# Kernel optimization log

Hardware: AMD Instinct MI355X
Metric: run time of the kernel (lower is better)

The kernel has to match this reference:

```python
import jax, jax.numpy as jnp
import numpy as np

B = 256            # number of graphs
N_NODES = 512      # nodes per graph
D = 128            # embedding_dim = hidden_dim
NUM_EDGE_CLASSES = 8
N_TOTAL = B * N_NODES
N_EDGES = N_TOTAL * 8   # avg degree 8
EDGES_DIM = N_NODES * (N_NODES - 1) // 2


def _ln(x, g, b):
    m = jnp.mean(x, axis=-1, keepdims=True)
    v = jnp.var(x, axis=-1, keepdims=True)
    return (x - m) * jax.lax.rsqrt(v + 1e-5) * g + b


def _mlp_ln(x, W1, b1, g, be, W2, b2):
    # MLP(input,hidden,output, n_hidden_layers=1, add_layer_norm=True):
    # Linear -> LayerNorm -> ReLU -> Linear
    return jax.nn.relu(_ln(x @ W1 + b1, g, be)) @ W2 + b2


def setup_inputs() -> dict:
    key = jax.random.key(0)
    ks = jax.random.split(key, 12)
    s = 1.0 / np.sqrt(D)
    return {
        "node_features": jax.random.randint(ks[0], (N_TOTAL, 1), 0, N_NODES),
        "edge_index": jax.random.randint(ks[1], (2, N_EDGES), 0, N_TOTAL),
        "batch_ptr": jnp.arange(B + 1, dtype=jnp.int32) * N_NODES,
        "emb": jax.random.normal(ks[2], (N_NODES, D), jnp.float32) * 0.02,
        "gin_W1": jax.random.normal(ks[3], (D, D), jnp.float32) * s,
        "gin_b1": jnp.zeros((D,), jnp.float32),
        "gin_g1": jnp.ones((D,), jnp.float32),
        "gin_be1": jnp.zeros((D,), jnp.float32),
        "gin_W2": jax.random.normal(ks[4], (D, D), jnp.float32) * s,
        "gin_b2": jnp.zeros((D,), jnp.float32),
        "post_W1": jax.random.normal(ks[5], (D, D), jnp.float32) * s,
        "post_b1": jnp.zeros((D,), jnp.float32),
        "post_W2": jax.random.normal(ks[6], (D, D), jnp.float32) * s,
        "post_b2": jnp.zeros((D,), jnp.float32),
        "norm_g": jnp.ones((D,), jnp.float32),
        "norm_b": jnp.zeros((D,), jnp.float32),
        "exit_W1": jax.random.normal(ks[7], (D, D), jnp.float32) * s,
        "exit_b1": jnp.zeros((D,), jnp.float32),
        "exit_g": jnp.ones((D,), jnp.float32),
        "exit_be": jnp.zeros((D,), jnp.float32),
        "exit_W2": jax.random.normal(ks[8], (D, 1), jnp.float32) * s,
        "exit_b2": jnp.zeros((1,), jnp.float32),
    }


def reference(node_features, edge_index, batch_ptr, emb,
              gin_W1, gin_b1, gin_g1, gin_be1, gin_W2, gin_b2,
              post_W1, post_b1, post_W2, post_b2,
              norm_g, norm_b,
              exit_W1, exit_b1, exit_g, exit_be, exit_W2, exit_b2):
    # node embedding lookup
    x = emb[node_features.squeeze(-1)]                      # [N_total, D]

    # single GIN conv layer (eps=0): MLP(x + sum_{j in N(i)} x_j)
    src, dst = edge_index[0], edge_index[1]
    agg = jax.ops.segment_sum(x[src], dst, num_segments=N_TOTAL)
    h = _mlp_ln(x + agg, gin_W1, gin_b1, gin_g1, gin_be1, gin_W2, gin_b2)
    # post-conv Sequential(Linear, ReLU, Linear)
    h = jax.nn.relu(h @ post_W1 + post_b1) @ post_W2 + post_b2
    # i == 0: no residual; then LayerNorm
    x = _ln(h, norm_g, norm_b)                              # [N_total, D]

    # segment mean via cumsum (faithful to _group_mean)
    cs = jnp.concatenate([jnp.zeros((1, D), x.dtype), jnp.cumsum(x, axis=0)], 0)
    sizes = (batch_ptr[1:] - batch_ptr[:-1]).astype(x.dtype)
    means = (cs[batch_ptr[1:]] - cs[batch_ptr[:-1]]) / sizes[:, None]  # [B, D]

    exit_action = _mlp_ln(means, exit_W1, exit_b1, exit_g, exit_be,
                          exit_W2, exit_b2).squeeze(-1)     # [B]

    # per-graph pairwise dot products, upper-triangular gather
    xb = x.reshape(B, N_NODES, D)
    scores = jnp.einsum('bnf,bmf->bnm', xb, xb) / jnp.sqrt(
        jnp.asarray(D, x.dtype))                            # [B, n, n]
    iu, ju = jnp.triu_indices(N_NODES, k=1)
    edge_actions = scores[:, iu, ju]                        # [B, EDGES_DIM]

    # action_type: index 1 = ADD_EDGE, 2 = EXIT (GraphActionType assumption)
    action_type = (jnp.zeros((B, 3), x.dtype)
                   .at[:, 1].set(1.0 - exit_action)
                   .at[:, 2].set(exit_action))
    edge_class = jnp.zeros((B, NUM_EDGE_CLASSES), x.dtype)
    node_class = jnp.zeros((B, 1), x.dtype)
    return (action_type, edge_class, node_class, edge_actions)
```

## Files before the change

kernel.cpp:

```cpp
#include <hip/hip_runtime.h>
#include <hip/hip_bf16.h>

#define NBATCH 256
#define NNODES 512
#define DIM    128
#define NTOT   (NBATCH*NNODES)
#define NEDGE  (NTOT*8)
#define EPB    130816
#define CAP    32

typedef __attribute__((ext_vector_type(8))) short  short8;
typedef __attribute__((ext_vector_type(4))) float  f32x4;

__device__ __forceinline__ unsigned short f2bf(float f){
  unsigned u = __builtin_bit_cast(unsigned, f);
  unsigned r = u + 0x7FFFu + ((u >> 16) & 1u);
  return (unsigned short)(r >> 16);
}

__global__ __launch_bounds__(256) void k_prep(
    const float* __restrict__ emb, const float* __restrict__ W1,
    unsigned short* __restrict__ embW1,
    const float* __restrict__ W2, const float* __restrict__ P1,
    const float* __restrict__ P2, unsigned short* __restrict__ wswz,
    int* __restrict__ cnt, float* __restrict__ gsum, float* __restrict__ out)
{
  const int tid = threadIdx.x;
  const int blk = blockIdx.x;
  __shared__ float er[2][DIM];
  if (blk < 256) {
    const int half = tid >> 7, c = tid & 127;
    const int r = blk*2 + half;
    er[half][c] = emb[r*DIM + c];
    __syncthreads();
    float acc = 0.f;
    #pragma unroll 8
    for (int k = 0; k < DIM; ++k) acc = fmaf(er[half][k], W1[k*DIM + c], acc);
    embW1[r*DIM + c] = f2bf(acc);
  } else if (blk < 448) {
    int idx = (blk - 256)*256 + tid;
    int s = idx >> 14, rem = idx & 16383;
    int ks = rem >> 12, n = (rem >> 9) & 7, lane = (rem >> 3) & 63, j = rem & 7;
    int lg = lane >> 4, l15 = lane & 15;
    int k = ks*32 + lg*8 + j, c = n*16 + l15;
    const float* src = (s == 0) ? W2 : ((s == 1) ? P1 : P2);
    wswz[idx] = f2bf(src[k*DIM + c]);
  } else {
    int idx = (blk - 448)*256 + tid;
    if (idx < NTOT)                cnt[idx] = 0;
    else if (idx < NTOT + 32768)   gsum[idx - NTOT] = 0.f;
    else                           out[idx - NTOT - 32768] = 0.f;
  }
}

__global__ __launch_bounds__(256) void k_edges(const int* __restrict__ ei,
                                               const int* __restrict__ nf,
                                               int* __restrict__ cnt,
                                               unsigned short* __restrict__ slots){
  const int base = (blockIdx.x >> 3)*4096 + threadIdx.x;
  const int r    = blockIdx.x & 7;
  #pragma unroll
  for (int it = 0; it < 16; ++it) {
    const int e = base + it*256;
    const int d = ei[NEDGE + e];
    if ((d >> 14) == r) {
      const int s = ei[e];
      const int v = nf[s];
      const int pos = atomicAdd(&cnt[d], 1);
      if (pos < CAP) slots[(size_t)d*CAP + pos] = (unsigned short)v;
    }
  }
}

__global__ __launch_bounds__(512, 4) void k_gnn(
    const unsigned short* __restrict__ embW1, const int* __restrict__ nf,
    const int* __restrict__ cnt, const unsigned short* __restrict__ slots,
    const float* __restrict__ b1, const float* __restrict__ g1,
    const float* __restrict__ be1,
    const unsigned short* __restrict__ wswz,
    const float* __restrict__ b2,  const float* __restrict__ pb1, const float* __restrict__ pb2,
    const float* __restrict__ ng,  const float* __restrict__ nbv,
    unsigned short* __restrict__ xbuf, float* __restrict__ gsum)
{
  __shared__ unsigned short act[32][136];
  __shared__ float rpart[4][32][2];
  __shared__ float rfin[32][2];
  __shared__ float gpart[8][128];
  const int tid   = threadIdx.x;
  const int nbase = blockIdx.x * 32;

  {
    const int node = nbase + (tid >> 4);
    const int part = tid & 15;
    const short8* base8 = (const short8*)embW1;

    const int self = nf[node];
    int m = cnt[node]; if (m > CAP) m = CAP;
    const unsigned short* sl = slots + (size_t)node*CAP;
    const uint4 sv0 = *(const uint4*)(sl);
    const uint4 sv1 = *(const uint4*)(sl + 8);
    const uint4 sv2 = *(const uint4*)(sl + 16);
    unsigned sw[12] = {sv0.x,sv0.y,sv0.z,sv0.w, sv1.x,sv1.y,sv1.z,sv1.w,
                       sv2.x,sv2.y,sv2.z,sv2.w};

    float a[8];
    {
      const float4* bp = (const float4*)(b1 + part*8);
      float4 x = bp[0], y = bp[1];
      a[0]=x.x; a[1]=x.y; a[2]=x.z; a[3]=x.w;
      a[4]=y.x; a[5]=y.y; a[6]=y.z; a[7]=y.w;
    }
#define ACC8(V) { _Pragma("unroll") \
    for (int i_ = 0; i_ < 8; ++i_) { \
      unsigned uu = ((unsigned)(unsigned short)(V)[i_]) << 16; \
      a[i_] += __builtin_bit_cast(float, uu); } }

    {
      short8 t0 = base8[(size_t)self*16 + part];
      short8 t[8];
      #pragma unroll
      for (int e = 0; e < 8; ++e) {
        unsigned id = (sw[e >> 1] >> ((e & 1)*16)) & 0xffffu;
        int idx = (e < m) ? (int)id : self;
        t[e] = base8[(size_t)idx*16 + part];
      }
      ACC8(t0)
      #pragma unroll
      for (int e = 0; e < 8; ++e) if (e < m) ACC8(t[e])
    }
    if (m > 8) {
      short8 t[8];
      #pragma unroll
      for (int e = 0; e < 8; ++e) {
        unsigned id = (sw[4 + (e >> 1)] >> ((e & 1)*16)) & 0xffffu;
        int idx = (e + 8 < m) ? (int)id : self;
        t[e] = base8[(size_t)idx*16 + part];
      }
      #pragma unroll
      for (int e = 0; e < 8; ++e) if (e + 8 < m) ACC8(t[e])
    }
    if (m > 16) {
      short8 t[8];
      #pragma unroll
      for (int e = 0; e < 8; ++e) {
        unsigned id = (sw[8 + (e >> 1)] >> ((e & 1)*16)) & 0xffffu;
        int idx = (e + 16 < m) ? (int)id : self;
        t[e] = base8[(size_t)idx*16 + part];
      }
      #pragma unroll
      for (int e = 0; e < 8; ++e) if (e + 16 < m) ACC8(t[e])
    }
    for (int e = 24; e < m; ++e) {
      short8 t = base8[(size_t)sl[e]*16 + part];
      ACC8(t)
    }

    float s = 0.f, qs = 0.f;
    #pragma unroll
    for (int i = 0; i < 8; ++i) { s += a[i]; qs += a[i]*a[i]; }
    #pragma unroll
    for (int msk = 1; msk < 16; msk <<= 1) {
      s  += __shfl_xor(s,  msk, 64);
      qs += __shfl_xor(qs, msk, 64);
    }
    const float mean = s * (1.f/128.f);
    const float var  = qs * (1.f/128.f) - mean*mean;
    const float rs   = rsqrtf(var + 1e-5f);
    float gg[8], bb[8];
    {
      const float4* gp = (const float4*)(g1  + part*8);
      const float4* ep = (const float4*)(be1 + part*8);
      float4 g0 = gp[0], g1v = gp[1], e0 = ep[0], e1v = ep[1];
      gg[0]=g0.x; gg[1]=g0.y; gg[2]=g0.z; gg[3]=g0.w;
      gg[4]=g1v.x; gg[5]=g1v.y; gg[6]=g1v.z; gg[7]=g1v.w;
      bb[0]=e0.x; bb[1]=e0.y; bb[2]=e0.z; bb[3]=e0.w;
      bb[4]=e1v.x; bb[5]=e1v.y; bb[6]=e1v.z; bb[7]=e1v.w;
    }
    float v[8];
    #pragma unroll
    for (int i = 0; i < 8; ++i)
      v[i] = fmaxf((a[i] - mean)*rs*gg[i] + bb[i], 0.f);
    uint4 pk;
    pk.x = (unsigned)f2bf(v[0]) | ((unsigned)f2bf(v[1]) << 16);
    pk.y = (unsigned)f2bf(v[2]) | ((unsigned)f2bf(v[3]) << 16);
    pk.z = (unsigned)f2bf(v[4]) | ((unsigned)f2bf(v[5]) << 16);
    pk.w = (unsigned)f2bf(v[6]) | ((unsigned)f2bf(v[7]) << 16);
    *(uint4*)&act[tid >> 4][part*8] = pk;
  }
  __syncthreads();

  const int wave = tid >> 6, lane = tid & 63;
  const int l15 = lane & 15, lg = lane >> 4;
  const int rt = wave & 1, nb = wave >> 1;
  const int arow = rt*16 + l15;
  const short8* ws8 = (const short8*)wswz;

  for (int s = 0; s < 3; ++s) {
    f32x4 acc0 = (f32x4){0.f,0.f,0.f,0.f};
    f32x4 acc1 = (f32x4){0.f,0.f,0.f,0.f};
    #pragma unroll
    for (int ks = 0; ks < 4; ++ks) {
      short8 af  = *(const short8*)&act[arow][ks*32 + lg*8];
      short8 bf0 = ws8[s*2048 + ks*512 + (nb*2 + 0)*64 + lane];
      short8 bf1 = ws8[s*2048 + ks*512 + (nb*2 + 1)*64 + lane];
      acc0 = __builtin_amdgcn_mfma_f32_16x16x32_bf16(af, bf0, acc0, 0, 0, 0);
      acc1 = __builtin_amdgcn_mfma_f32_16x16x32_bf16(af, bf1, acc1, 0, 0, 0);
    }
    __syncthreads();

    if (s < 2) {
      const float* bias = (s == 0) ? b2 : pb1;
      const float bb0 = bias[nb*32 + l15], bb1 = bias[nb*32 + 16 + l15];
      #pragma unroll
      for (int q = 0; q < 4; ++q) {
        float x0 = acc0[q] + bb0, x1 = acc1[q] + bb1;
        if (s == 1) { x0 = fmaxf(x0, 0.f); x1 = fmaxf(x1, 0.f); }
        act[rt*16 + lg*4 + q][nb*32 + l15]      = f2bf(x0);
        act[rt*16 + lg*4 + q][nb*32 + 16 + l15] = f2bf(x1);
      }
      __syncthreads();
    } else {
      const float bb0 = pb2[nb*32 + l15], bb1 = pb2[nb*32 + 16 + l15];
      float w0v[4], w1v[4], sr[4], qr[4];
      #pragma unroll
      for (int q = 0; q < 4; ++q) {
        float x0 = acc0[q] + bb0, x1 = acc1[q] + bb1;
        w0v[q] = x0; w1v[q] = x1;
        sr[q] = x0 + x1; qr[q] = x0*x0 + x1*x1;
      }
      #pragma unroll
      for (int msk = 1; msk < 16; msk <<= 1) {
        #pragma unroll
        for (int q = 0; q < 4; ++q) {
          sr[q] += __shfl_xor(sr[q], msk, 64);
          qr[q] += __shfl_xor(qr[q], msk, 64);
        }
      }
      if (l15 == 0) {
        #pragma unroll
        for (int q = 0; q < 4; ++q) {
          rpart[nb][rt*16 + lg*4 + q][0] = sr[q];
          rpart[nb][rt*16 + lg*4 + q][1] = qr[q];
        }
      }
      __syncthreads();
      if (tid < 64) {
        int row = tid >> 1, vv = tid & 1;
        rfin[row][vv] = rpart[0][row][vv] + rpart[1][row][vv]
                      + rpart[2][row][vv] + rpart[3][row][vv];
      }
      __syncthreads();
      const int c0 = nb*32 + l15, c1 = c0 + 16;
      const float gc0 = ng[c0], gc1 = ng[c1], bc0 = nbv[c0], bc1 = nbv[c1];
      float pc0 = 0.f, pc1 = 0.f;
      #pragma unroll
      for (int q = 0; q < 4; ++q) {
        const int row = rt*16 + lg*4 + q;
        const float mean = rfin[row][0]*(1.f/128.f);
        const float var  = rfin[row][1]*(1.f/128.f) - mean*mean;
        const float rs   = rsqrtf(var + 1e-5f);
        float x0 = (w0v[q] - mean)*rs*gc0 + bc0;
        float x1 = (w1v[q] - mean)*rs*gc1 + bc1;
        act[row][c0] = f2bf(x0);
        act[row][c1] = f2bf(x1);
        pc0 += x0; pc1 += x1;
      }
      pc0 += __shfl_xor(pc0, 16, 64); pc0 += __shfl_xor(pc0, 32, 64);
      pc1 += __shfl_xor(pc1, 16, 64); pc1 += __shfl_xor(pc1, 32, 64);
      if (lg == 0) { gpart[wave][c0] = pc0; gpart[wave][c1] = pc1; }
      __syncthreads();
      if (tid < 128) {
        const int w0 = (tid >> 5)*2;
        float s2 = gpart[w0][tid] + gpart[w0 + 1][tid];
        atomicAdd(&gsum[(blockIdx.x >> 4)*DIM + tid], s2);
      }
      {
        short8* xs8 = (short8*)xbuf;
        const int i = tid;
        const int rowgrp = i >> 8, rem = i & 255;
        const int kc = rem >> 4, lv = rem & 15;
        short8 vv = *(const short8*)&act[rowgrp*16 + lv][kc*8];
        xs8[((size_t)(nbase >> 4) + rowgrp)*256 + kc*16 + lv] = vv;
      }
    }
  }
}

__global__ __launch_bounds__(256) void k_scores(const unsigned short* __restrict__ xswz,
    const float* __restrict__ gsum,
    const float* __restrict__ eW1, const float* __restrict__ eb1,
    const float* __restrict__ eg,  const float* __restrict__ ebe,
    const float* __restrict__ eW2, const float* __restrict__ eb2,
    float* __restrict__ out)
{
  const int tid = threadIdx.x;

  if (blockIdx.x >= 2560) {
    __shared__ float mrow[2][DIM];
    __shared__ float red[2][2][2];
    __shared__ float red2[2][2];
    const int grp = tid >> 7;
    const int t   = tid & 127;
    const int gi  = ((int)blockIdx.x - 2560)*2 + grp;
    mrow[grp][t] = gsum[gi*DIM + t] * (1.f/512.f);
    __syncthreads();
    float u = eb1[t];
    #pragma unroll 8
    for (int k = 0; k < DIM; ++k) u = fmaf(mrow[grp][k], eW1[k*DIM + t], u);
    float s = u, q = u*u;
    #pragma unroll
    for (int m = 1; m < 64; m <<= 1) { s += __shfl_xor(s, m, 64); q += __shfl_xor(q, m, 64); }
    const int wv = (tid >> 6) & 1;
    if ((tid & 63) == 0) { red[grp][wv][0] = s; red[grp][wv][1] = q; }
    __syncthreads();
    const float S = red[grp][0][0] + red[grp][1][0];
    const float Q = red[grp][0][1] + red[grp][1][1];
    const float mean = S*(1.f/128.f);
    const float var  = Q*(1.f/128.f) - mean*mean;
    float av = fmaxf((u - mean)*rsqrtf(var + 1e-5f)*eg[t] + ebe[t], 0.f);
    float p = av * eW2[t];
    #pragma unroll
    for (int m = 1; m < 64; m <<= 1) p += __shfl_xor(p, m, 64);
    if ((tid & 63) == 0) red2[grp][wv] = p;
    __syncthreads();
    if (t == 0) {
      float e = red2[grp][0] + red2[grp][1] + eb2[0];
      out[gi*3 + 1] = 1.f - e;
      out[gi*3 + 2] = e;
    }
    return;
  }

  static const int TI[10] = {0,0,0,0,1,1,1,2,2,3};
  static const int TJ[10] = {0,1,2,3,1,2,3,2,3,3};
  const int b = blockIdx.x & 255, p = blockIdx.x >> 8;
  const int ti = TI[p], tj = TJ[p];
  const int wave = tid >> 6, lane = tid & 63;
  const int l15 = lane & 15, lg = lane >> 4;
  const short8* Xs = (const short8*)xswz + (size_t)b*8192;

  f32x4 acc0[8], acc1[8];
  #pragma unroll
  for (int n = 0; n < 8; ++n) { acc0[n] = (f32x4){0,0,0,0}; acc1[n] = (f32x4){0,0,0,0}; }

  #pragma unroll
  for (int ks = 0; ks < 4; ++ks) {
    const int kq = ks*4 + lg;
    short8 a0 = Xs[(size_t)(ti*8 + wave*2 + 0)*256 + kq*16 + l15];
    short8 a1 = Xs[(size_t)(ti*8 + wave*2 + 1)*256 + kq*16 + l15];
    #pragma unroll
    for (int n = 0; n < 8; ++n) {
      short8 bf = Xs[(size_t)(tj*8 + n)*256 + kq*16 + l15];
      acc0[n] = __builtin_amdgcn_mfma_f32_16x16x32_bf16(a0, bf, acc0[n], 0, 0, 0);
      acc1[n] = __builtin_amdgcn_mfma_f32_16x16x32_bf16(a1, bf, acc1[n], 0, 0, 0);
    }
  }

  const float scale = 0.08838834764831845f;
  float* ea = out + 3072 + (size_t)b*EPB;
  #pragma unroll
  for (int m = 0; m < 2; ++m) {
    #pragma unroll
    for (int n = 0; n < 8; ++n) {
      const int gj = tj*128 + n*16 + l15;
      #pragma unroll
      for (int r = 0; r < 4; ++r) {
        const int gi = ti*128 + wave*32 + m*16 + lg*4 + r;
        if (gi < gj) {
          const int rowbase = gi*511 - (gi*(gi-1))/2 - gi - 1;
          const float v = (m == 0) ? acc0[n][r] : acc1[n][r];
          ea[rowbase + gj] = v * scale;
        }
      }
    }
  }
}

extern "C" void kernel_launch(void* const* d_in, const int* in_sizes, int n_in,
                              void* d_out, int out_size, void* d_ws, size_t ws_size,
                              hipStream_t stream) {
  const int*   nf   = (const int*)d_in[0];
  const int*   ei   = (const int*)d_in[1];
  const float* emb  = (const float*)d_in[3];
  const float* gW1  = (const float*)d_in[4];
  const float* gb1  = (const float*)d_in[5];
  const float* gg1  = (const float*)d_in[6];
  const float* gbe1 = (const float*)d_in[7];
  const float* gW2  = (const float*)d_in[8];
  const float* gb2  = (const float*)d_in[9];
  const float* pW1  = (const float*)d_in[10];
  const float* pb1  = (const float*)d_in[11];
  const float* pW2  = (const float*)d_in[12];
  const float* pb2  = (const float*)d_in[13];
  const float* ng   = (const float*)d_in[14];
  const float* nb   = (const float*)d_in[15];
  const float* eW1  = (const float*)d_in[16];
  const float* eb1  = (const float*)d_in[17];
  const float* eg   = (const float*)d_in[18];
  const float* ebe  = (const float*)d_in[19];
  const float* eW2  = (const float*)d_in[20];
  const float* eb2  = (const float*)d_in[21];
  float* out = (float*)d_out;

  char* ws = (char*)d_ws;
  unsigned short* embW1 = (unsigned short*)ws;
  unsigned short* wswz  = (unsigned short*)(ws + 262144);
  int*            cnt   = (int*)(ws + 360448);
  unsigned short* slots = (unsigned short*)(ws + 884736);
  unsigned short* xbuf  = (unsigned short*)(ws + 13467648);
  float*          gsum  = (float*)(ws + 47022080);
  if (ws_size < 47153152) return;

  k_prep  <<<1100, 256, 0, stream>>>(emb, gW1, embW1, gW2, pW1, pW2, wswz,
                                     cnt, gsum, out);
  k_edges <<<2048, 256, 0, stream>>>(ei, nf, cnt, slots);
  k_gnn   <<<4096, 512, 0, stream>>>(embW1, nf, cnt, slots, gb1, gg1, gbe1,
                                     wswz, gb2, pb1, pb2, ng, nb, xbuf, gsum);
  k_scores<<<2688, 256, 0, stream>>>(xbuf, gsum, eW1, eb1, eg, ebe, eW2, eb2, out);
}
```

Measured before the change: 164.9 us.

## Fuse GNN MLP, graph mean, exit head and pairwise scores into one per-graph kernel

Merges k_gnn and k_scores into a single kernel that runs one 512-thread block per graph. Each block keeps all 512 node embeddings in shared memory (about 136 KB), runs the three MLP stages over the whole graph, reduces the graph mean locally instead of with global atomics, evaluates the exit head, and computes the upper-triangular pairwise scores straight from shared memory. This removes the xbuf round trip through global memory, the gsum atomics and zeroing, and one launch. In exchange only 256 blocks run on the GPU, with heavy register and shared-memory use per block, so occupancy and parallelism drop sharply. Because the score phase is bound by output writes, that lost parallelism may cost more than the traffic saved.

```diff
diff --git a/kernel.cpp b/kernel.cpp
--- a/kernel.cpp
+++ b/kernel.cpp
@@ -23,7 +23,7 @@
     unsigned short* __restrict__ embW1,
     const float* __restrict__ W2, const float* __restrict__ P1,
     const float* __restrict__ P2, unsigned short* __restrict__ wswz,
-    int* __restrict__ cnt, float* __restrict__ gsum, float* __restrict__ out)
+    int* __restrict__ cnt)
 {
   const int tid = threadIdx.x;
   const int blk = blockIdx.x;
@@ -46,10 +46,7 @@
     const float* src = (s == 0) ? W2 : ((s == 1) ? P1 : P2);
     wswz[idx] = f2bf(src[k*DIM + c]);
   } else {
-    int idx = (blk - 448)*256 + tid;
-    if (idx < NTOT)                cnt[idx] = 0;
-    else if (idx < NTOT + 32768)   gsum[idx - NTOT] = 0.f;
-    else                           out[idx - NTOT - 32768] = 0.f;
+    cnt[(blk - 448)*256 + tid] = 0;
   }
 }
 
@@ -72,7 +69,7 @@
   }
 }
 
-__global__ __launch_bounds__(512, 4) void k_gnn(
+__global__ __launch_bounds__(512, 2) void k_mega(
     const unsigned short* __restrict__ embW1, const int* __restrict__ nf,
     const int* __restrict__ cnt, const unsigned short* __restrict__ slots,
     const float* __restrict__ b1, const float* __restrict__ g1,
@@ -80,296 +77,288 @@
     const unsigned short* __restrict__ wswz,
     const float* __restrict__ b2,  const float* __restrict__ pb1, const float* __restrict__ pb2,
     const float* __restrict__ ng,  const float* __restrict__ nbv,
-    unsigned short* __restrict__ xbuf, float* __restrict__ gsum)
-{
-  __shared__ unsigned short act[32][136];
-  __shared__ float rpart[4][32][2];
-  __shared__ float rfin[32][2];
-  __shared__ float gpart[8][128];
-  const int tid   = threadIdx.x;
-  const int nbase = blockIdx.x * 32;
-
-  {
-    const int node = nbase + (tid >> 4);
-    const int part = tid & 15;
-    const short8* base8 = (const short8*)embW1;
-
-    const int self = nf[node];
-    int m = cnt[node]; if (m > CAP) m = CAP;
-    const unsigned short* sl = slots + (size_t)node*CAP;
-    const uint4 sv0 = *(const uint4*)(sl);
-    const uint4 sv1 = *(const uint4*)(sl + 8);
-    const uint4 sv2 = *(const uint4*)(sl + 16);
-    unsigned sw[12] = {sv0.x,sv0.y,sv0.z,sv0.w, sv1.x,sv1.y,sv1.z,sv1.w,
-                       sv2.x,sv2.y,sv2.z,sv2.w};
-
-    float a[8];
-    {
-      const float4* bp = (const float4*)(b1 + part*8);
-      float4 x = bp[0], y = bp[1];
-      a[0]=x.x; a[1]=x.y; a[2]=x.z; a[3]=x.w;
-      a[4]=y.x; a[5]=y.y; a[6]=y.z; a[7]=y.w;
-    }
-#define ACC8(V) { _Pragma("unroll") \
-    for (int i_ = 0; i_ < 8; ++i_) { \
-      unsigned uu = ((unsigned)(unsigned short)(V)[i_]) << 16; \
-      a[i_] += __builtin_bit_cast(float, uu); } }
-
-    {
-      short8 t0 = base8[(size_t)self*16 + part];
-      short8 t[8];
-      #pragma unroll
-      for (int e = 0; e < 8; ++e) {
-        unsigned id = (sw[e >> 1] >> ((e & 1)*16)) & 0xffffu;
-        int idx = (e < m) ? (int)id : self;
-        t[e] = base8[(size_t)idx*16 + part];
-      }
-      ACC8(t0)
-      #pragma unroll
-      for (int e = 0; e < 8; ++e) if (e < m) ACC8(t[e])
-    }
-    if (m > 8) {
-      short8 t[8];
-      #pragma unroll
-      for (int e = 0; e < 8; ++e) {
-        unsigned id = (sw[4 + (e >> 1)] >> ((e & 1)*16)) & 0xffffu;
-        int idx = (e + 8 < m) ? (int)id : self;
-        t[e] = base8[(size_t)idx*16 + part];
-      }
-      #pragma unroll
-      for (int e = 0; e < 8; ++e) if (e + 8 < m) ACC8(t[e])
-    }
-    if (m > 16) {
-      short8 t[8];
-      #pragma unroll
-      for (int e = 0; e < 8; ++e) {
-        unsigned id = (sw[8 + (e >> 1)] >> ((e & 1)*16)) & 0xffffu;
-        int idx = (e + 16 < m) ? (int)id : self;
-        t[e] = base8[(size_t)idx*16 + part];
-      }
-      #pragma unroll
-      for (int e = 0; e < 8; ++e) if (e + 16 < m) ACC8(t[e])
-    }
-    for (int e = 24; e < m; ++e) {
-      short8 t = base8[(size_t)sl[e]*16 + part];
-      ACC8(t)
-    }
-
-    float s = 0.f, qs = 0.f;
-    #pragma unroll
-    for (int i = 0; i < 8; ++i) { s += a[i]; qs += a[i]*a[i]; }
-    #pragma unroll
-    for (int msk = 1; msk < 16; msk <<= 1) {
-      s  += __shfl_xor(s,  msk, 64);
-      qs += __shfl_xor(qs, msk, 64);
-    }
-    const float mean = s * (1.f/128.f);
-    const float var  = qs * (1.f/128.f) - mean*mean;
-    const float rs   = rsqrtf(var + 1e-5f);
-    float gg[8], bb[8];
-    {
-      const float4* gp = (const float4*)(g1  + part*8);
-      const float4* ep = (const float4*)(be1 + part*8);
-      float4 g0 = gp[0], g1v = gp[1], e0 = ep[0], e1v = ep[1];
-      gg[0]=g0.x; gg[1]=g0.y; gg[2]=g0.z; gg[3]=g0.w;
-      gg[4]=g1v.x; gg[5]=g1v.y; gg[6]=g1v.z; gg[7]=g1v.w;
-      bb[0]=e0.x; bb[1]=e0.y; bb[2]=e0.z; bb[3]=e0.w;
-      bb[4]=e1v.x; bb[5]=e1v.y; bb[6]=e1v.z; bb[7]=e1v.w;
-    }
-    float v[8];
-    #pragma unroll
-    for (int i = 0; i < 8; ++i)
-      v[i] = fmaxf((a[i] - mean)*rs*gg[i] + bb[i], 0.f);
-    uint4 pk;
-    pk.x = (unsigned)f2bf(v[0]) | ((unsigned)f2bf(v[1]) << 16);
-    pk.y = (unsigned)f2bf(v[2]) | ((unsigned)f2bf(v[3]) << 16);
-    pk.z = (unsigned)f2bf(v[4]) | ((unsigned)f2bf(v[5]) << 16);
-    pk.w = (unsigned)f2bf(v[6]) | ((unsigned)f2bf(v[7]) << 16);
-    *(uint4*)&act[tid >> 4][part*8] = pk;
-  }
-  __syncthreads();
-
-  const int wave = tid >> 6, lane = tid & 63;
-  const int l15 = lane & 15, lg = lane >> 4;
-  const int rt = wave & 1, nb = wave >> 1;
-  const int arow = rt*16 + l15;
-  const short8* ws8 = (const short8*)wswz;
-
-  for (int s = 0; s < 3; ++s) {
-    f32x4 acc0 = (f32x4){0.f,0.f,0.f,0.f};
-    f32x4 acc1 = (f32x4){0.f,0.f,0.f,0.f};
-    #pragma unroll
-    for (int ks = 0; ks < 4; ++ks) {
-      short8 af  = *(const short8*)&act[arow][ks*32 + lg*8];
-      short8 bf0 = ws8[s*2048 + ks*512 + (nb*2 + 0)*64 + lane];
-      short8 bf1 = ws8[s*2048 + ks*512 + (nb*2 + 1)*64 + lane];
-      acc0 = __builtin_amdgcn_mfma_f32_16x16x32_bf16(af, bf0, acc0, 0, 0, 0);
-      acc1 = __builtin_amdgcn_mfma_f32_16x16x32_bf16(af, bf1, acc1, 0, 0, 0);
-    }
-    __syncthreads();
-
-    if (s < 2) {
-      const float* bias = (s == 0) ? b2 : pb1;
-      const float bb0 = bias[nb*32 + l15], bb1 = bias[nb*32 + 16 + l15];
-      #pragma unroll
-      for (int q = 0; q < 4; ++q) {
-        float x0 = acc0[q] + bb0, x1 = acc1[q] + bb1;
-        if (s == 1) { x0 = fmaxf(x0, 0.f); x1 = fmaxf(x1, 0.f); }
-        act[rt*16 + lg*4 + q][nb*32 + l15]      = f2bf(x0);
-        act[rt*16 + lg*4 + q][nb*32 + 16 + l15] = f2bf(x1);
-      }
-      __syncthreads();
-    } else {
-      const float bb0 = pb2[nb*32 + l15], bb1 = pb2[nb*32 + 16 + l15];
-      float w0v[4], w1v[4], sr[4], qr[4];
-      #pragma unroll
-      for (int q = 0; q < 4; ++q) {
-        float x0 = acc0[q] + bb0, x1 = acc1[q] + bb1;
-        w0v[q] = x0; w1v[q] = x1;
-        sr[q] = x0 + x1; qr[q] = x0*x0 + x1*x1;
-      }
-      #pragma unroll
-      for (int msk = 1; msk < 16; msk <<= 1) {
-        #pragma unroll
-        for (int q = 0; q < 4; ++q) {
-          sr[q] += __shfl_xor(sr[q], msk, 64);
-          qr[q] += __shfl_xor(qr[q], msk, 64);
-        }
-      }
-      if (l15 == 0) {
-        #pragma unroll
-        for (int q = 0; q < 4; ++q) {
-          rpart[nb][rt*16 + lg*4 + q][0] = sr[q];
-          rpart[nb][rt*16 + lg*4 + q][1] = qr[q];
-        }
-      }
-      __syncthreads();
-      if (tid < 64) {
-        int row = tid >> 1, vv = tid & 1;
-        rfin[row][vv] = rpart[0][row][vv] + rpart[1][row][vv]
-                      + rpart[2][row][vv] + rpart[3][row][vv];
-      }
-      __syncthreads();
-      const int c0 = nb*32 + l15, c1 = c0 + 16;
-      const float gc0 = ng[c0], gc1 = ng[c1], bc0 = nbv[c0], bc1 = nbv[c1];
-      float pc0 = 0.f, pc1 = 0.f;
-      #pragma unroll
-      for (int q = 0; q < 4; ++q) {
-        const int row = rt*16 + lg*4 + q;
-        const float mean = rfin[row][0]*(1.f/128.f);
-        const float var  = rfin[row][1]*(1.f/128.f) - mean*mean;
-        const float rs   = rsqrtf(var + 1e-5f);
-        float x0 = (w0v[q] - mean)*rs*gc0 + bc0;
-        float x1 = (w1v[q] - mean)*rs*gc1 + bc1;
-        act[row][c0] = f2bf(x0);
-        act[row][c1] = f2bf(x1);
-        pc0 += x0; pc1 += x1;
-      }
-      pc0 += __shfl_xor(pc0, 16, 64); pc0 += __shfl_xor(pc0, 32, 64);
-      pc1 += __shfl_xor(pc1, 16, 64); pc1 += __shfl_xor(pc1, 32, 64);
-      if (lg == 0) { gpart[wave][c0] = pc0; gpart[wave][c1] = pc1; }
-      __syncthreads();
-      if (tid < 128) {
-        const int w0 = (tid >> 5)*2;
-        float s2 = gpart[w0][tid] + gpart[w0 + 1][tid];
-        atomicAdd(&gsum[(blockIdx.x >> 4)*DIM + tid], s2);
-      }
-      {
-        short8* xs8 = (short8*)xbuf;
-        const int i = tid;
-        const int rowgrp = i >> 8, rem = i & 255;
-        const int kc = rem >> 4, lv = rem & 15;
-        short8 vv = *(const short8*)&act[rowgrp*16 + lv][kc*8];
-        xs8[((size_t)(nbase >> 4) + rowgrp)*256 + kc*16 + lv] = vv;
-      }
-    }
-  }
-}
-
-__global__ __launch_bounds__(256) void k_scores(const unsigned short* __restrict__ xswz,
-    const float* __restrict__ gsum,
     const float* __restrict__ eW1, const float* __restrict__ eb1,
     const float* __restrict__ eg,  const float* __restrict__ ebe,
     const float* __restrict__ eW2, const float* __restrict__ eb2,
     float* __restrict__ out)
 {
-  const int tid = threadIdx.x;
-
-  if (blockIdx.x >= 2560) {
-    __shared__ float mrow[2][DIM];
-    __shared__ float red[2][2][2];
-    __shared__ float red2[2][2];
-    const int grp = tid >> 7;
-    const int t   = tid & 127;
-    const int gi  = ((int)blockIdx.x - 2560)*2 + grp;
-    mrow[grp][t] = gsum[gi*DIM + t] * (1.f/512.f);
-    __syncthreads();
-    float u = eb1[t];
+  __shared__ unsigned short X[512][136];
+  __shared__ float gpart[8][128];
+  __shared__ float mrow[128];
+  __shared__ float redA[4];
+  __shared__ float redB[2];
+  const int tid   = threadIdx.x;
+  const int bb    = blockIdx.x;
+  const int nbase = bb * NNODES;
+
+  {
+    const int part = tid & 15;
+    const short8* base8 = (const short8*)embW1;
+    #pragma unroll 1
+    for (int pass = 0; pass < 16; ++pass) {
+      const int lnode = pass*32 + (tid >> 4);
+      const int node  = nbase + lnode;
+      const int self = nf[node];
+      int m = cnt[node]; if (m > CAP) m = CAP;
+      const unsigned short* sl = slots + (size_t)node*CAP;
+      const uint4 sv0 = *(const uint4*)(sl);
+      const uint4 sv1 = *(const uint4*)(sl + 8);
+      const uint4 sv2 = *(const uint4*)(sl + 16);
+      unsigned sw[12] = {sv0.x,sv0.y,sv0.z,sv0.w, sv1.x,sv1.y,sv1.z,sv1.w,
+                         sv2.x,sv2.y,sv2.z,sv2.w};
+      float a[8];
+      {
+        const float4* bp = (const float4*)(b1 + part*8);
+        float4 x = bp[0], y = bp[1];
+        a[0]=x.x; a[1]=x.y; a[2]=x.z; a[3]=x.w;
+        a[4]=y.x; a[5]=y.y; a[6]=y.z; a[7]=y.w;
+      }
+#define ACC8(V) { _Pragma("unroll") \
+      for (int i_ = 0; i_ < 8; ++i_) { \
+        unsigned uu = ((unsigned)(unsigned short)(V)[i_]) << 16; \
+        a[i_] += __builtin_bit_cast(float, uu); } }
+      {
+        short8 t0 = base8[(size_t)self*16 + part];
+        short8 t[8];
+        #pragma unroll
+        for (int e = 0; e < 8; ++e) {
+          unsigned id = (sw[e >> 1] >> ((e & 1)*16)) & 0xffffu;
+          int idx = (e < m) ? (int)id : self;
+          t[e] = base8[(size_t)idx*16 + part];
+        }
+        ACC8(t0)
+        #pragma unroll
+        for (int e = 0; e < 8; ++e) if (e < m) ACC8(t[e])
+      }
+      if (m > 8) {
+        short8 t[8];
+        #pragma unroll
+        for (int e = 0; e < 8; ++e) {
+          unsigned id = (sw[4 + (e >> 1)] >> ((e & 1)*16)) & 0xffffu;
+          int idx = (e + 8 < m) ? (int)id : self;
+          t[e] = base8[(size_t)idx*16 + part];
+        }
+        #pragma unroll
+        for (int e = 0; e < 8; ++e) if (e + 8 < m) ACC8(t[e])
+      }
+      if (m > 16) {
+        short8 t[8];
+        #pragma unroll
+        for (int e = 0; e < 8; ++e) {
+          unsigned id = (sw[8 + (e >> 1)] >> ((e & 1)*16)) & 0xffffu;
+          int idx = (e + 16 < m) ? (int)id : self;
+          t[e] = base8[(size_t)idx*16 + part];
+        }
+        #pragma unroll
+        for (int e = 0; e < 8; ++e) if (e + 16 < m) ACC8(t[e])
+      }
+      for (int e = 24; e < m; ++e) {
+        short8 t = base8[(size_t)sl[e]*16 + part];
+        ACC8(t)
+      }
+      float s = 0.f, qs = 0.f;
+      #pragma unroll
+      for (int i = 0; i < 8; ++i) { s += a[i]; qs += a[i]*a[i]; }
+      #pragma unroll
+      for (int msk = 1; msk < 16; msk <<= 1) {
+        s  += __shfl_xor(s,  msk, 64);
+        qs += __shfl_xor(qs, msk, 64);
+      }
+      const float mean = s * (1.f/128.f);
+      const float var  = qs * (1.f/128.f) - mean*mean;
+      const float rs   = rsqrtf(var + 1e-5f);
+      const float4* gp = (const float4*)(g1  + part*8);
+      const float4* ep = (const float4*)(be1 + part*8);
+      float4 g0 = gp[0], g1v = gp[1], e0 = ep[0], e1v = ep[1];
+      float gg[8] = {g0.x,g0.y,g0.z,g0.w, g1v.x,g1v.y,g1v.z,g1v.w};
+      float eb[8] = {e0.x,e0.y,e0.z,e0.w, e1v.x,e1v.y,e1v.z,e1v.w};
+      float v[8];
+      #pragma unroll
+      for (int i = 0; i < 8; ++i)
+        v[i] = fmaxf((a[i] - mean)*rs*gg[i] + eb[i], 0.f);
+      uint4 pk;
+      pk.x = (unsigned)f2bf(v[0]) | ((unsigned)f2bf(v[1]) << 16);
+      pk.y = (unsigned)f2bf(v[2]) | ((unsigned)f2bf(v[3]) << 16);
+      pk.z = (unsigned)f2bf(v[4]) | ((unsigned)f2bf(v[5]) << 16);
+      pk.w = (unsigned)f2bf(v[6]) | ((unsigned)f2bf(v[7]) << 16);
+      *(uint4*)&X[lnode][part*8] = pk;
+    }
+  }
+  __syncthreads();
+
+  const int wave = tid >> 6, lane = tid & 63;
+  const int l15 = lane & 15, lg = lane >> 4;
+  const short8* ws8 = (const short8*)wswz;
+  float pc[8];
+  #pragma unroll
+  for (int n = 0; n < 8; ++n) pc[n] = 0.f;
+
+  #pragma unroll
+  for (int s = 0; s < 3; ++s) {
+    f32x4 acc[4][8];
+    #pragma unroll
+    for (int p4 = 0; p4 < 4; ++p4)
+      #pragma unroll
+      for (int n = 0; n < 8; ++n) acc[p4][n] = (f32x4){0.f,0.f,0.f,0.f};
+    #pragma unroll
+    for (int ks = 0; ks < 4; ++ks) {
+      short8 bf[8];
+      #pragma unroll
+      for (int n = 0; n < 8; ++n) bf[n] = ws8[s*2048 + ks*512 + n*64 + lane];
+      #pragma unroll
+      for (int p4 = 0; p4 < 4; ++p4) {
+        short8 af = *(const short8*)&X[p4*128 + wave*16 + l15][ks*32 + lg*8];
+        #pragma unroll
+        for (int n = 0; n < 8; ++n)
+          acc[p4][n] = __builtin_amdgcn_mfma_f32_16x16x32_bf16(af, bf[n], acc[p4][n], 0, 0, 0);
+      }
+    }
+    if (s < 2) {
+      const float* bias = (s == 0) ? b2 : pb1;
+      float bv[8];
+      #pragma unroll
+      for (int n = 0; n < 8; ++n) bv[n] = bias[n*16 + l15];
+      #pragma unroll
+      for (int p4 = 0; p4 < 4; ++p4)
+        #pragma unroll
+        for (int n = 0; n < 8; ++n)
+          #pragma unroll
+          for (int q = 0; q < 4; ++q) {
+            float v = acc[p4][n][q] + bv[n];
+            if (s == 1) v = fmaxf(v, 0.f);
+            X[p4*128 + wave*16 + lg*4 + q][n*16 + l15] = f2bf(v);
+          }
+    } else {
+      float bv[8], gc[8], bc[8];
+      #pragma unroll
+      for (int n = 0; n < 8; ++n) {
+        bv[n] = pb2[n*16 + l15];
+        gc[n] = ng [n*16 + l15];
+        bc[n] = nbv[n*16 + l15];
+      }
+      #pragma unroll
+      for (int p4 = 0; p4 < 4; ++p4) {
+        float sr[4] = {0,0,0,0}, qr[4] = {0,0,0,0};
+        #pragma unroll
+        for (int n = 0; n < 8; ++n)
+          #pragma unroll
+          for (int q = 0; q < 4; ++q) {
+            float v = acc[p4][n][q] + bv[n];
+            acc[p4][n][q] = v;
+            sr[q] += v; qr[q] += v*v;
+          }
+        #pragma unroll
+        for (int msk = 1; msk < 16; msk <<= 1)
+          #pragma unroll
+          for (int q = 0; q < 4; ++q) {
+            sr[q] += __shfl_xor(sr[q], msk, 64);
+            qr[q] += __shfl_xor(qr[q], msk, 64);
+          }
+        float mean[4], rs[4];
+        #pragma unroll
+        for (int q = 0; q < 4; ++q) {
+          mean[q] = sr[q]*(1.f/128.f);
+          float var = qr[q]*(1.f/128.f) - mean[q]*mean[q];
+          rs[q] = rsqrtf(var + 1e-5f);
+        }
+        #pragma unroll
+        for (int n = 0; n < 8; ++n)
+          #pragma unroll
+          for (int q = 0; q < 4; ++q) {
+            float xo = (acc[p4][n][q] - mean[q])*rs[q]*gc[n] + bc[n];
+            X[p4*128 + wave*16 + lg*4 + q][n*16 + l15] = f2bf(xo);
+            pc[n] += xo;
+          }
+      }
+    }
+  }
+  #pragma unroll
+  for (int n = 0; n < 8; ++n) {
+    pc[n] += __shfl_xor(pc[n], 16, 64);
+    pc[n] += __shfl_xor(pc[n], 32, 64);
+  }
+  if (lg == 0) {
+    #pragma unroll
+    for (int n = 0; n < 8; ++n) gpart[wave][n*16 + l15] = pc[n];
+  }
+  __syncthreads();
+
+  if (tid < 128) {
+    float m = 0.f;
+    #pragma unroll
+    for (int w = 0; w < 8; ++w) m += gpart[w][tid];
+    mrow[tid] = m * (1.f/512.f);
+  }
+  __syncthreads();
+  float uu = 0.f;
+  if (tid < 128) {
+    uu = eb1[tid];
     #pragma unroll 8
-    for (int k = 0; k < DIM; ++k) u = fmaf(mrow[grp][k], eW1[k*DIM + t], u);
-    float s = u, q = u*u;
-    #pragma unroll
-    for (int m = 1; m < 64; m <<= 1) { s += __shfl_xor(s, m, 64); q += __shfl_xor(q, m, 64); }
-    const int wv = (tid >> 6) & 1;
-    if ((tid & 63) == 0) { red[grp][wv][0] = s; red[grp][wv][1] = q; }
-    __syncthreads();
-    const float S = red[grp][0][0] + red[grp][1][0];
-    const float Q = red[grp][0][1] + red[grp][1][1];
+    for (int k = 0; k < DIM; ++k) uu = fmaf(mrow[k], eW1[k*DIM + tid], uu);
+    float s2 = uu, q2 = uu*uu;
+    #pragma unroll
+    for (int msk = 1; msk < 64; msk <<= 1) {
+      s2 += __shfl_xor(s2, msk, 64); q2 += __shfl_xor(q2, msk, 64);
+    }
+    if ((tid & 63) == 0) { redA[(tid >> 6)*2] = s2; redA[(tid >> 6)*2 + 1] = q2; }
+  }
+  __syncthreads();
+  if (tid < 128) {
+    const float S = redA[0] + redA[2], Q = redA[1] + redA[3];
     const float mean = S*(1.f/128.f);
     const float var  = Q*(1.f/128.f) - mean*mean;
-    float av = fmaxf((u - mean)*rsqrtf(var + 1e-5f)*eg[t] + ebe[t], 0.f);
-    float p = av * eW2[t];
-    #pragma unroll
-    for (int m = 1; m < 64; m <<= 1) p += __shfl_xor(p, m, 64);
-    if ((tid & 63) == 0) red2[grp][wv] = p;
-    __syncthreads();
-    if (t == 0) {
-      float e = red2[grp][0] + red2[grp][1] + eb2[0];
-      out[gi*3 + 1] = 1.f - e;
-      out[gi*3 + 2] = e;
-    }
-    return;
-  }
-
-  static const int TI[10] = {0,0,0,0,1,1,1,2,2,3};
-  static const int TJ[10] = {0,1,2,3,1,2,3,2,3,3};
-  const int b = blockIdx.x & 255, p = blockIdx.x >> 8;
-  const int ti = TI[p], tj = TJ[p];
-  const int wave = tid >> 6, lane = tid & 63;
-  const int l15 = lane & 15, lg = lane >> 4;
-  const short8* Xs = (const short8*)xswz + (size_t)b*8192;
-
-  f32x4 acc0[8], acc1[8];
-  #pragma unroll
-  for (int n = 0; n < 8; ++n) { acc0[n] = (f32x4){0,0,0,0}; acc1[n] = (f32x4){0,0,0,0}; }
-
-  #pragma unroll
-  for (int ks = 0; ks < 4; ++ks) {
-    const int kq = ks*4 + lg;
-    short8 a0 = Xs[(size_t)(ti*8 + wave*2 + 0)*256 + kq*16 + l15];
-    short8 a1 = Xs[(size_t)(ti*8 + wave*2 + 1)*256 + kq*16 + l15];
-    #pragma unroll
-    for (int n = 0; n < 8; ++n) {
-      short8 bf = Xs[(size_t)(tj*8 + n)*256 + kq*16 + l15];
-      acc0[n] = __builtin_amdgcn_mfma_f32_16x16x32_bf16(a0, bf, acc0[n], 0, 0, 0);
-      acc1[n] = __builtin_amdgcn_mfma_f32_16x16x32_bf16(a1, bf, acc1[n], 0, 0, 0);
-    }
-  }
-
+    float av = fmaxf((uu - mean)*rsqrtf(var + 1e-5f)*eg[tid] + ebe[tid], 0.f);
+    float p = av * eW2[tid];
+    #pragma unroll
+    for (int msk = 1; msk < 64; msk <<= 1) p += __shfl_xor(p, msk, 64);
+    if ((tid & 63) == 0) redB[tid >> 6] = p;
+  }
+  __syncthreads();
+  if (tid == 0) {
+    float e = redB[0] + redB[1] + eb2[0];
+    out[bb*3 + 0] = 0.f;
+    out[bb*3 + 1] = 1.f - e;
+    out[bb*3 + 2] = e;
+  }
+  if (tid < 8)   out[768 + bb*8 + tid] = 0.f;
+  if (tid == 8)  out[2816 + bb] = 0.f;
+
+  float* ea = out + 3072 + (size_t)bb*EPB;
   const float scale = 0.08838834764831845f;
-  float* ea = out + 3072 + (size_t)b*EPB;
-  #pragma unroll
-  for (int m = 0; m < 2; ++m) {
-    #pragma unroll
-    for (int n = 0; n < 8; ++n) {
-      const int gj = tj*128 + n*16 + l15;
-      #pragma unroll
-      for (int r = 0; r < 4; ++r) {
-        const int gi = ti*128 + wave*32 + m*16 + lg*4 + r;
-        if (gi < gj) {
-          const int rowbase = gi*511 - (gi*(gi-1))/2 - gi - 1;
-          const float v = (m == 0) ? acc0[n][r] : acc1[n][r];
-          ea[rowbase + gj] = v * scale;
+  #pragma unroll 1
+  for (int i = 0; i < 5; ++i) {
+    const int task = wave*5 + i;
+    const int p  = task >> 2, rg = task & 3;
+    const int ti = (int)((0x3221110000ULL >> (p*4)) & 0xF);
+    const int tj = (int)((0x3323213210ULL >> (p*4)) & 0xF);
+    f32x4 acc0[8], acc1[8];
+    #pragma unroll
+    for (int n = 0; n < 8; ++n) { acc0[n] = (f32x4){0,0,0,0}; acc1[n] = (f32x4){0,0,0,0}; }
+    #pragma unroll
+    for (int ks = 0; ks < 4; ++ks) {
+      const int k0 = ks*32 + lg*8;
+      short8 a0 = *(const short8*)&X[ti*128 + rg*32 +      l15][k0];
+      short8 a1 = *(const short8*)&X[ti*128 + rg*32 + 16 + l15][k0];
+      #pragma unroll
+      for (int n = 0; n < 8; ++n) {
+        short8 bf = *(const short8*)&X[tj*128 + n*16 + l15][k0];
+        acc0[n] = __builtin_amdgcn_mfma_f32_16x16x32_bf16(a0, bf, acc0[n], 0, 0, 0);
+        acc1[n] = __builtin_amdgcn_mfma_f32_16x16x32_bf16(a1, bf, acc1[n], 0, 0, 0);
+      }
+    }
+    #pragma unroll
+    for (int m = 0; m < 2; ++m) {
+      #pragma unroll
+      for (int n = 0; n < 8; ++n) {
+        const int gj = tj*128 + n*16 + l15;
+        #pragma unroll
+        for (int r = 0; r < 4; ++r) {
+          const int gi = ti*128 + rg*32 + m*16 + lg*4 + r;
+          if (gi < gj) {
+            const int rowbase = gi*511 - (gi*(gi-1))/2 - gi - 1;
+            const float v = (m == 0) ? acc0[n][r] : acc1[n][r];
+            ea[rowbase + gj] = v * scale;
+          }
         }
       }
     }
@@ -407,14 +396,11 @@
   unsigned short* wswz  = (unsigned short*)(ws + 262144);
   int*            cnt   = (int*)(ws + 360448);
   unsigned short* slots = (unsigned short*)(ws + 884736);
-  unsigned short* xbuf  = (unsigned short*)(ws + 13467648);
-  float*          gsum  = (float*)(ws + 47022080);
-  if (ws_size < 47153152) return;
-
-  k_prep  <<<1100, 256, 0, stream>>>(emb, gW1, embW1, gW2, pW1, pW2, wswz,
-                                     cnt, gsum, out);
+  if (ws_size < 9273344) return;
+
+  k_prep  <<<960,  256, 0, stream>>>(emb, gW1, embW1, gW2, pW1, pW2, wswz, cnt);
   k_edges <<<2048, 256, 0, stream>>>(ei, nf, cnt, slots);
-  k_gnn   <<<4096, 512, 0, stream>>>(embW1, nf, cnt, slots, gb1, gg1, gbe1,
-                                     wswz, gb2, pb1, pb2, ng, nb, xbuf, gsum);
-  k_scores<<<2688, 256, 0, stream>>>(xbuf, gsum, eW1, eb1, eg, ebe, eW2, eb2, out);
+  k_mega  <<<256,  512, 0, stream>>>(embW1, nf, cnt, slots, gb1, gg1, gbe1,
+                                     wswz, gb2, pb1, pb2, ng, nb,
+                                     eW1, eb1, eg, ebe, eW2, eb2, out);
 }
```

Result: faster. 150.3 us (-8.8%).

## Transpose score tile for vectorized row stores, fold scale into bf16 activations

Applied to the files above, without the earlier changes.

The final node activations are multiplied by D^-1/4 before the bf16 cast, so the pairwise dot products come out already scaled and the separate multiply disappears. The MFMA operands are swapped so each lane holds four consecutive columns of one row. The upper-triangle output can then be written with float4 stores instead of scattered scalar stores. Each wave now handles its row groups in two passes, skips sub-tiles below the diagonal in diagonal tiles, and the kernel adds an occupancy hint in launch bounds. The float4 stores can land on addresses that are not 16-byte aligned, which relies on the hardware tolerating unaligned vector stores. Folding the scale into bf16 also changes rounding slightly.

```diff
diff --git a/kernel.cpp b/kernel.cpp
--- a/kernel.cpp
+++ b/kernel.cpp
@@ -88,6 +88,7 @@
   __shared__ float gpart[8][128];
   const int tid   = threadIdx.x;
   const int nbase = blockIdx.x * 32;
+  const float PRESCL = 0.29730177875068026f;
 
   {
     const int node = nbase + (tid >> 4);
@@ -261,8 +262,8 @@
         const float rs   = rsqrtf(var + 1e-5f);
         float x0 = (w0v[q] - mean)*rs*gc0 + bc0;
         float x1 = (w1v[q] - mean)*rs*gc1 + bc1;
-        act[row][c0] = f2bf(x0);
-        act[row][c1] = f2bf(x1);
+        act[row][c0] = f2bf(x0 * PRESCL);
+        act[row][c1] = f2bf(x1 * PRESCL);
         pc0 += x0; pc1 += x1;
       }
       pc0 += __shfl_xor(pc0, 16, 64); pc0 += __shfl_xor(pc0, 32, 64);
@@ -286,7 +287,7 @@
   }
 }
 
-__global__ __launch_bounds__(256) void k_scores(const unsigned short* __restrict__ xswz,
+__global__ __launch_bounds__(256, 6) void k_scores(const unsigned short* __restrict__ xswz,
     const float* __restrict__ gsum,
     const float* __restrict__ eW1, const float* __restrict__ eb1,
     const float* __restrict__ eg,  const float* __restrict__ ebe,
@@ -331,46 +332,50 @@
     return;
   }
 
-  static const int TI[10] = {0,0,0,0,1,1,1,2,2,3};
-  static const int TJ[10] = {0,1,2,3,1,2,3,2,3,3};
   const int b = blockIdx.x & 255, p = blockIdx.x >> 8;
-  const int ti = TI[p], tj = TJ[p];
+  const int ti = (int)((0x3221110000ULL >> (p*4)) & 0xF);
+  const int tj = (int)((0x3323213210ULL >> (p*4)) & 0xF);
+  const bool diag = (ti == tj);
   const int wave = tid >> 6, lane = tid & 63;
   const int l15 = lane & 15, lg = lane >> 4;
   const short8* Xs = (const short8*)xswz + (size_t)b*8192;
-
-  f32x4 acc0[8], acc1[8];
-  #pragma unroll
-  for (int n = 0; n < 8; ++n) { acc0[n] = (f32x4){0,0,0,0}; acc1[n] = (f32x4){0,0,0,0}; }
-
-  #pragma unroll
-  for (int ks = 0; ks < 4; ++ks) {
-    const int kq = ks*4 + lg;
-    short8 a0 = Xs[(size_t)(ti*8 + wave*2 + 0)*256 + kq*16 + l15];
-    short8 a1 = Xs[(size_t)(ti*8 + wave*2 + 1)*256 + kq*16 + l15];
+  float* ea = out + 3072 + (size_t)b*EPB;
+
+  #pragma unroll 1
+  for (int pass = 0; pass < 2; ++pass) {
+    const int rg  = pass*4 + wave;
+    const int nlo = diag ? rg : 0;
+
+    f32x4 acc[8];
+    #pragma unroll
+    for (int n = 0; n < 8; ++n) acc[n] = (f32x4){0,0,0,0};
+    #pragma unroll
+    for (int ks = 0; ks < 4; ++ks) {
+      const int kq = ks*4 + lg;
+      short8 bfrag = Xs[(size_t)(ti*8 + rg)*256 + kq*16 + l15];
+      #pragma unroll
+      for (int n = 0; n < 8; ++n) {
+        if (n >= nlo) {
+          short8 afrag = Xs[(size_t)(tj*8 + n)*256 + kq*16 + l15];
+          acc[n] = __builtin_amdgcn_mfma_f32_16x16x32_bf16(afrag, bfrag, acc[n], 0, 0, 0);
+        }
+      }
+    }
+    const int lgi = rg*16 + l15;
+    const int gi  = ti*128 + lgi;
+    const int rowbase = gi*511 - ((gi*(gi-1)) >> 1) - gi - 1;
+    float* rowp = ea + rowbase + tj*128;
     #pragma unroll
     for (int n = 0; n < 8; ++n) {
-      short8 bf = Xs[(size_t)(tj*8 + n)*256 + kq*16 + l15];
-      acc0[n] = __builtin_amdgcn_mfma_f32_16x16x32_bf16(a0, bf, acc0[n], 0, 0, 0);
-      acc1[n] = __builtin_amdgcn_mfma_f32_16x16x32_bf16(a1, bf, acc1[n], 0, 0, 0);
-    }
-  }
-
-  const float scale = 0.08838834764831845f;
-  float* ea = out + 3072 + (size_t)b*EPB;
-  #pragma unroll
-  for (int m = 0; m < 2; ++m) {
-    #pragma unroll
-    for (int n = 0; n < 8; ++n) {
-      const int gj = tj*128 + n*16 + l15;
-      #pragma unroll
-      for (int r = 0; r < 4; ++r) {
-        const int gi = ti*128 + wave*32 + m*16 + lg*4 + r;
-        if (gi < gj) {
-          const int rowbase = gi*511 - (gi*(gi-1))/2 - gi - 1;
-          const float v = (m == 0) ? acc0[n][r] : acc1[n][r];
-          ea[rowbase + gj] = v * scale;
-        }
+      if (n < nlo) continue;
+      const int lgj = n*16 + lg*4;
+      float4 v = make_float4(acc[n][0], acc[n][1], acc[n][2], acc[n][3]);
+      if (!diag || lgj > lgi) {
+        *(float4*)(rowp + lgj) = v;
+      } else if (lgj + 3 > lgi) {
+        #pragma unroll
+        for (int j = 1; j < 4; ++j)
+          if (lgj + j > lgi) rowp[lgj + j] = acc[n][j];
       }
     }
   }
```

After: 217.2 us. 1.32x slower.
